# Performance work log

Hardware: AMD Instinct MI355X
Metric: run time of the kernel (lower is better)

## Reference

```python
import jax, jax.numpy as jnp
import numpy as np

DECAY = 0.99
EPS = 1e-05
COMMIT = 0.25


def setup_inputs() -> dict:
    key = jax.random.key(0)
    k1, k2 = jax.random.split(key)
    dim, n_embed = 256, 8192
    z = jax.random.normal(k1, (32, 32, 32, dim), dtype=jnp.float32)
    embed = jax.random.normal(k2, (dim, n_embed), dtype=jnp.float32)
    cluster_size = jnp.zeros((n_embed,), dtype=jnp.float32)
    embed_avg = embed  # torch init: embed_avg = embed.clone()
    return {"z": z, "embed": embed, "cluster_size": cluster_size, "embed_avg": embed_avg}


def reference(z, embed, cluster_size, embed_avg):
    dim, n_embed = embed.shape
    flatten = z.reshape(-1, dim)                       # [N, D]
    # squared L2 distance to each code: ||f||^2 - 2 f.E + ||E||^2
    dist = ((flatten ** 2).sum(1, keepdims=True)
            - 2.0 * flatten @ embed
            + (embed ** 2).sum(0, keepdims=True))      # [N, K]
    ind = jnp.argmin(dist, axis=1)                     # [N]
    quantize = jnp.take(embed.T, ind, axis=0).reshape(z.shape)
    embed_ind = ind.reshape(z.shape[:-1])

    # EMA codebook update (training mode), via segment_sum instead of a dense one-hot
    counts = jax.ops.segment_sum(jnp.ones_like(ind, dtype=flatten.dtype), ind,
                                 num_segments=n_embed)          # [K]
    embed_sum = jax.ops.segment_sum(flatten, ind,
                                    num_segments=n_embed).T     # [D, K]
    cluster_size_new = cluster_size * DECAY + (1.0 - DECAY) * counts
    embed_avg_new = embed_avg * DECAY + (1.0 - DECAY) * embed_sum
    n = cluster_size_new.sum()
    cs = (cluster_size_new + EPS) / (n + n_embed * EPS) * n
    embed_new = embed_avg_new / cs[None, :]

    diff = COMMIT * jnp.mean((jax.lax.stop_gradient(quantize) - z) ** 2)
    quantize_st = z + jax.lax.stop_gradient(quantize - z)  # straight-through
    return quantize_st, diff, embed_ind, embed_new
```

## Files before the change

### kernel.cpp

```cpp
#include <hip/hip_runtime.h>
#include <hip/hip_bf16.h>

#define D 256
#define K 8192
#define NTOT 32768
#define BM 128
#define BN2 128
#define BD 32
#define CSPLIT 4
#define CT_PER (K / CSPLIT / BN2)

typedef __bf16 bf16x8 __attribute__((ext_vector_type(8)));
typedef float f32x4 __attribute__((ext_vector_type(4)));

__device__ __forceinline__ void gl_lds16(const void* g, void* l) {
    __builtin_amdgcn_global_load_lds(
        (__attribute__((address_space(1))) void*)(g),
        (__attribute__((address_space(3))) void*)(l), 16, 0, 0);
}

__device__ __forceinline__ unsigned int enc_f32(float f) {
    unsigned int u = __float_as_uint(f);
    return (u & 0x80000000u) ? ~u : (u | 0x80000000u);
}

__device__ __forceinline__ unsigned short f2bfu(float x) {
    __hip_bfloat16 h = __float2bfloat16(x);
    return __builtin_bit_cast(unsigned short, h);
}
__device__ __forceinline__ float bfu2f(unsigned short u) {
    return __bfloat162float(__builtin_bit_cast(__hip_bfloat16, u));
}

__global__ __launch_bounds__(256)
void conv_F(const float* __restrict__ z, unsigned short* __restrict__ Fhi,
            unsigned short* __restrict__ Flo) {
    int i4 = blockIdx.x * 256 + threadIdx.x;
    float4 v = ((const float4*)z)[i4];
    ushort4 h, l;
    h.x = f2bfu(v.x); l.x = f2bfu(v.x - bfu2f(h.x));
    h.y = f2bfu(v.y); l.y = f2bfu(v.y - bfu2f(h.y));
    h.z = f2bfu(v.z); l.z = f2bfu(v.z - bfu2f(h.z));
    h.w = f2bfu(v.w); l.w = f2bfu(v.w - bfu2f(h.w));
    ((ushort4*)Fhi)[i4] = h;
    ((ushort4*)Flo)[i4] = l;
}

__global__ __launch_bounds__(256)
void conv_E(const float* __restrict__ E, unsigned short* __restrict__ EhiT,
            unsigned short* __restrict__ EloT, float* __restrict__ ET,
            float* __restrict__ enorm) {
    __shared__ float tile[64][65];
    int tid = threadIdx.x;
    int k0 = blockIdx.x * 64, d0 = blockIdx.y * 64;
#pragma unroll
    for (int it = 0; it < 16; ++it) {
        int idx = it * 256 + tid;
        int dr = idx >> 6, kc = idx & 63;
        tile[kc][dr] = E[(d0 + dr) * K + k0 + kc];
    }
    __syncthreads();
    float psum[4];
#pragma unroll
    for (int it = 0; it < 16; ++it) {
        int idx = it * 256 + tid;
        int kr = idx >> 6, dc = idx & 63;
        float v = tile[kr][dc];
        unsigned short h = f2bfu(v);
        int o = (k0 + kr) * D + d0 + dc;
        EhiT[o] = h;
        EloT[o] = f2bfu(v - bfu2f(h));
        ET[o] = v;
        psum[it & 3] = (it < 4 ? 0.f : psum[it & 3]) + v * v;
    }
#pragma unroll
    for (int g = 0; g < 4; ++g) {
        float p = psum[g];
#pragma unroll
        for (int off = 32; off; off >>= 1) p += __shfl_down(p, off);
        if ((tid & 63) == 0) {
            int kr = g * 4 + (tid >> 6);
            atomicAdd(&enorm[k0 + kr * 4 + 0], 0.f);
        }
    }
}

__global__ __launch_bounds__(256)
void enorm_kernel(const float* __restrict__ ET, float* __restrict__ enorm) {
    int k = blockIdx.x * 256 + threadIdx.x;
    const float4* row = (const float4*)(ET + k * D);
    float s = 0.f;
#pragma unroll
    for (int d = 0; d < D / 4; ++d) {
        float4 v = row[d];
        s += v.x * v.x + v.y * v.y + v.z * v.z + v.w * v.w;
    }
    enorm[k] = s;
}

__global__ __launch_bounds__(256)
void mfma_dist_argmin(const unsigned short* __restrict__ Fhi,
                      const unsigned short* __restrict__ Flo,
                      const unsigned short* __restrict__ EhiT,
                      const unsigned short* __restrict__ EloT,
                      const float* __restrict__ enorm,
                      unsigned long long* __restrict__ bestpack) {
    __shared__ unsigned short Ah[BM * BD], Al[BM * BD], Bh[BN2 * BD], Bl[BN2 * BD];

    const int tid = threadIdx.x;
    const int wave = tid >> 6;
    const int lane = tid & 63;
    const int qd = lane >> 4;
    const int ln = lane & 15;
    const int wm = (wave >> 1) * 64;
    const int wn = (wave & 1) * 64;
    const int n0 = blockIdx.x * BM;
    const int c0 = blockIdx.y * (K / CSPLIT);
    const int r_ = tid >> 2;
    const int s_sw = (tid & 3) ^ ((tid >> 3) & 3);
    const int csw = (qd ^ ((ln >> 1) & 3)) * 8;

    float bestv[16];
    int besti[16];
#pragma unroll
    for (int i = 0; i < 16; ++i) { bestv[i] = 3.402823466e38f; besti[i] = 0; }

    for (int ct = 0; ct < CT_PER; ++ct) {
        const int cb = c0 + ct * BN2;
        f32x4 acc[4][4];
#pragma unroll
        for (int mi = 0; mi < 4; ++mi)
#pragma unroll
            for (int ni = 0; ni < 4; ++ni) acc[mi][ni] = (f32x4){0.f, 0.f, 0.f, 0.f};

        for (int d0 = 0; d0 < D; d0 += BD) {
            __syncthreads();
#pragma unroll
            for (int it = 0; it < 2; ++it) {
                const int ga = (n0 + it * 64 + r_) * D + d0 + s_sw * 8;
                const int gb = (cb + it * 64 + r_) * D + d0 + s_sw * 8;
                const int lo = it * 2048 + wave * 512;
                gl_lds16(Fhi + ga, &Ah[lo]);
                gl_lds16(Flo + ga, &Al[lo]);
                gl_lds16(EhiT + gb, &Bh[lo]);
                gl_lds16(EloT + gb, &Bl[lo]);
            }
            __syncthreads();

            bf16x8 ah[4], al[4], bh[4], bl[4];
#pragma unroll
            for (int mi = 0; mi < 4; ++mi) {
                int off = (wm + mi * 16 + ln) * BD + csw;
                ah[mi] = *(const bf16x8*)&Ah[off];
                al[mi] = *(const bf16x8*)&Al[off];
            }
#pragma unroll
            for (int ni = 0; ni < 4; ++ni) {
                int off = (wn + ni * 16 + ln) * BD + csw;
                bh[ni] = *(const bf16x8*)&Bh[off];
                bl[ni] = *(const bf16x8*)&Bl[off];
            }
#pragma unroll
            for (int mi = 0; mi < 4; ++mi)
#pragma unroll
                for (int ni = 0; ni < 4; ++ni)
                    acc[mi][ni] = __builtin_amdgcn_mfma_f32_16x16x32_bf16(
                        ah[mi], bh[ni], acc[mi][ni], 0, 0, 0);
#pragma unroll
            for (int mi = 0; mi < 4; ++mi)
#pragma unroll
                for (int ni = 0; ni < 4; ++ni)
                    acc[mi][ni] = __builtin_amdgcn_mfma_f32_16x16x32_bf16(
                        ah[mi], bl[ni], acc[mi][ni], 0, 0, 0);
#pragma unroll
            for (int mi = 0; mi < 4; ++mi)
#pragma unroll
                for (int ni = 0; ni < 4; ++ni)
                    acc[mi][ni] = __builtin_amdgcn_mfma_f32_16x16x32_bf16(
                        al[mi], bh[ni], acc[mi][ni], 0, 0, 0);
        }

        float en[4];
#pragma unroll
        for (int ni = 0; ni < 4; ++ni) en[ni] = enorm[cb + wn + ni * 16 + ln];
#pragma unroll
        for (int ni = 0; ni < 4; ++ni) {
            int k = cb + wn + ni * 16 + ln;
#pragma unroll
            for (int mi = 0; mi < 4; ++mi) {
                f32x4 a = acc[mi][ni];
#pragma unroll
                for (int r = 0; r < 4; ++r) {
                    float dist = en[ni] - 2.0f * a[r];
                    int bi = mi * 4 + r;
                    if (dist < bestv[bi]) { bestv[bi] = dist; besti[bi] = k; }
                }
            }
        }
    }

#pragma unroll
    for (int mi = 0; mi < 4; ++mi) {
#pragma unroll
        for (int r = 0; r < 4; ++r) {
            int bi = mi * 4 + r;
            float v = bestv[bi];
            int ix = besti[bi];
#pragma unroll
            for (int off = 1; off < 16; off <<= 1) {
                float v2 = __shfl_xor(v, off);
                int i2 = __shfl_xor(ix, off);
                if (v2 < v || (v2 == v && i2 < ix)) { v = v2; ix = i2; }
            }
            if (ln == 0) {
                int m = n0 + wm + mi * 16 + qd * 4 + r;
                unsigned long long pack =
                    ((unsigned long long)enc_f32(v) << 32) | (unsigned int)ix;
                atomicMin(&bestpack[m], pack);
            }
        }
    }
}

#define ROWS_PER_BLOCK 64
__global__ __launch_bounds__(256)
void assign_apply(const float* __restrict__ z,
                  const float* __restrict__ ET,
                  const unsigned long long* __restrict__ bestpack,
                  float* __restrict__ out_q, float* __restrict__ out_ind,
                  float* __restrict__ out_diff,
                  float* __restrict__ counts, float* __restrict__ esumT) {
    const int tx = threadIdx.x;
    const int rbase = blockIdx.x * ROWS_PER_BLOCK;
    float part = 0.f;
    for (int r = 0; r < ROWS_PER_BLOCK; ++r) {
        int n = rbase + r;
        unsigned long long p = bestpack[n];
        int idx = (int)(p & 0xFFFFFFFFull);
        float f = z[n * D + tx];
        float q = ET[idx * D + tx];
        out_q[n * D + tx] = q;
        float dd = q - f;
        part += dd * dd;
        atomicAdd(&esumT[idx * D + tx], f);
        if (tx == 0) {
            atomicAdd(&counts[idx], 1.0f);
            out_ind[n] = (float)idx;
        }
    }
#pragma unroll
    for (int off = 32; off; off >>= 1) part += __shfl_down(part, off);
    __shared__ float wsum[4];
    if ((tx & 63) == 0) wsum[tx >> 6] = part;
    __syncthreads();
    if (tx == 0) {
        float t = wsum[0] + wsum[1] + wsum[2] + wsum[3];
        atomicAdd(out_diff, t * (0.25f / 8388608.0f));
    }
}

__global__ __launch_bounds__(1024)
void csn_sum(const float* __restrict__ cs_in, const float* __restrict__ counts,
             float* __restrict__ csn, float* __restrict__ nsum) {
    const float decay = 0.99f;
    const float omd = 0.01f;
    int tx = threadIdx.x;
    float p = 0.f;
    for (int k = tx; k < K; k += 1024) {
        float v = decay * cs_in[k] + omd * counts[k];
        csn[k] = v;
        p += v;
    }
#pragma unroll
    for (int off = 32; off; off >>= 1) p += __shfl_down(p, off);
    __shared__ float red[16];
    if ((tx & 63) == 0) red[tx >> 6] = p;
    __syncthreads();
    if (tx == 0) {
        float t = 0.f;
        for (int i = 0; i < 16; ++i) t += red[i];
        nsum[0] = t;
    }
}

__global__ __launch_bounds__(256)
void finalize(const float* __restrict__ eavg, const float* __restrict__ esumT,
              const float* __restrict__ csn, const float* __restrict__ nsum,
              float* __restrict__ out_enew) {
    const float decay = 0.99f;
    const float omd = 0.01f;
    const float keps = (float)(8192 * 1e-5);
    int idx = blockIdx.x * 256 + threadIdx.x;
    float nv = nsum[0];
    int k = idx & (K - 1);
    int d = idx >> 13;
    float avg_new = decay * eavg[idx] + omd * esumT[k * D + d];
    float cs = (csn[k] + 1e-5f) / (nv + keps) * nv;
    out_enew[idx] = avg_new / cs;
}

extern "C" void kernel_launch(void* const* d_in, const int* in_sizes, int n_in,
                              void* d_out, int out_size, void* d_ws, size_t ws_size,
                              hipStream_t stream) {
    const float* z = (const float*)d_in[0];
    const float* embed = (const float*)d_in[1];
    const float* cs_in = (const float*)d_in[2];
    const float* eavg = (const float*)d_in[3];

    float* out = (float*)d_out;
    float* out_q = out;
    float* out_diff = out + 8388608;
    float* out_ind = out + 8388609;
    float* out_enew = out + 8421377;

    char* ws = (char*)d_ws;
    unsigned long long* bestpack = (unsigned long long*)ws;
    float* enorm = (float*)(ws + 262144);
    float* counts = (float*)(ws + 294912);
    float* csn = (float*)(ws + 327680);
    float* nsum = (float*)(ws + 360448);
    float* esumT = (float*)(ws + 360704);
    unsigned short* Fhi = (unsigned short*)(ws + 8749312);
    unsigned short* Flo = (unsigned short*)(ws + 25526528);
    unsigned short* EhiT = (unsigned short*)(ws + 42303744);
    unsigned short* EloT = (unsigned short*)(ws + 46498048);
    float* ET = (float*)(ws + 50692352);

    hipMemsetAsync(bestpack, 0xFF, NTOT * 8, stream);
    hipMemsetAsync(counts, 0, K * 4, stream);
    hipMemsetAsync(esumT, 0, K * D * 4, stream);
    hipMemsetAsync(out_diff, 0, 4, stream);

    conv_F<<<NTOT * D / 4 / 256, 256, 0, stream>>>(z, Fhi, Flo);
    conv_E<<<dim3(K / 64, D / 64), 256, 0, stream>>>(embed, EhiT, EloT, ET, enorm);
    enorm_kernel<<<K / 256, 256, 0, stream>>>(ET, enorm);
    mfma_dist_argmin<<<dim3(NTOT / BM, CSPLIT), 256, 0, stream>>>(Fhi, Flo, EhiT, EloT,
                                                                  enorm, bestpack);
    assign_apply<<<NTOT / ROWS_PER_BLOCK, 256, 0, stream>>>(z, ET, bestpack, out_q,
                                                            out_ind, out_diff, counts, esumT);
    csn_sum<<<1, 1024, 0, stream>>>(cs_in, counts, csn, nsum);
    finalize<<<(D * K) / 256, 256, 0, stream>>>(eavg, esumT, csn, nsum, out_enew);
}
```

Measured before the change: 598.1 us.

## Load codebook fragments directly from global, shrink assign blocks, drop dead enorm atomics

In the distance GEMM kernel the B operand (codebook hi/lo bf16) is no longer staged through LDS. Each wave now reads its MFMA fragments straight from global memory into registers, which cuts LDS footprint and LDS traffic but duplicates global/L2 reads across the waves that share the same columns. Separately, conv_E drops its dead partial-norm reduction and zero-valued atomics, and assign_apply uses 16 rows per block with a partially unrolled loop to raise parallelism.

```diff
diff --git a/kernel.cpp b/kernel.cpp
--- a/kernel.cpp
+++ b/kernel.cpp
@@ -48,8 +48,7 @@
 
 __global__ __launch_bounds__(256)
 void conv_E(const float* __restrict__ E, unsigned short* __restrict__ EhiT,
-            unsigned short* __restrict__ EloT, float* __restrict__ ET,
-            float* __restrict__ enorm) {
+            unsigned short* __restrict__ EloT, float* __restrict__ ET) {
     __shared__ float tile[64][65];
     int tid = threadIdx.x;
     int k0 = blockIdx.x * 64, d0 = blockIdx.y * 64;
@@ -60,7 +59,6 @@
         tile[kc][dr] = E[(d0 + dr) * K + k0 + kc];
     }
     __syncthreads();
-    float psum[4];
 #pragma unroll
     for (int it = 0; it < 16; ++it) {
         int idx = it * 256 + tid;
@@ -71,17 +69,6 @@
         EhiT[o] = h;
         EloT[o] = f2bfu(v - bfu2f(h));
         ET[o] = v;
-        psum[it & 3] = (it < 4 ? 0.f : psum[it & 3]) + v * v;
-    }
-#pragma unroll
-    for (int g = 0; g < 4; ++g) {
-        float p = psum[g];
-#pragma unroll
-        for (int off = 32; off; off >>= 1) p += __shfl_down(p, off);
-        if ((tid & 63) == 0) {
-            int kr = g * 4 + (tid >> 6);
-            atomicAdd(&enorm[k0 + kr * 4 + 0], 0.f);
-        }
     }
 }
 
@@ -105,7 +92,7 @@
                       const unsigned short* __restrict__ EloT,
                       const float* __restrict__ enorm,
                       unsigned long long* __restrict__ bestpack) {
-    __shared__ unsigned short Ah[BM * BD], Al[BM * BD], Bh[BN2 * BD], Bl[BN2 * BD];
+    __shared__ unsigned short Ah[BM * BD], Al[BM * BD];
 
     const int tid = threadIdx.x;
     const int wave = tid >> 6;
@@ -120,6 +107,10 @@
     const int s_sw = (tid & 3) ^ ((tid >> 3) & 3);
     const int csw = (qd ^ ((ln >> 1) & 3)) * 8;
 
+    int boff[4];
+#pragma unroll
+    for (int ni = 0; ni < 4; ++ni) boff[ni] = (wn + ni * 16 + ln) * D + qd * 8;
+
     float bestv[16];
     int besti[16];
 #pragma unroll
@@ -138,27 +129,25 @@
 #pragma unroll
             for (int it = 0; it < 2; ++it) {
                 const int ga = (n0 + it * 64 + r_) * D + d0 + s_sw * 8;
-                const int gb = (cb + it * 64 + r_) * D + d0 + s_sw * 8;
                 const int lo = it * 2048 + wave * 512;
                 gl_lds16(Fhi + ga, &Ah[lo]);
                 gl_lds16(Flo + ga, &Al[lo]);
-                gl_lds16(EhiT + gb, &Bh[lo]);
-                gl_lds16(EloT + gb, &Bl[lo]);
+            }
+            const int sb = cb * D + d0;
+            bf16x8 bh[4], bl[4];
+#pragma unroll
+            for (int ni = 0; ni < 4; ++ni) {
+                bh[ni] = *(const bf16x8*)(EhiT + sb + boff[ni]);
+                bl[ni] = *(const bf16x8*)(EloT + sb + boff[ni]);
             }
             __syncthreads();
 
-            bf16x8 ah[4], al[4], bh[4], bl[4];
+            bf16x8 ah[4], al[4];
 #pragma unroll
             for (int mi = 0; mi < 4; ++mi) {
                 int off = (wm + mi * 16 + ln) * BD + csw;
                 ah[mi] = *(const bf16x8*)&Ah[off];
                 al[mi] = *(const bf16x8*)&Al[off];
-            }
-#pragma unroll
-            for (int ni = 0; ni < 4; ++ni) {
-                int off = (wn + ni * 16 + ln) * BD + csw;
-                bh[ni] = *(const bf16x8*)&Bh[off];
-                bl[ni] = *(const bf16x8*)&Bl[off];
             }
 #pragma unroll
             for (int mi = 0; mi < 4; ++mi)
@@ -222,7 +211,7 @@
     }
 }
 
-#define ROWS_PER_BLOCK 64
+#define ROWS_PER_BLOCK 16
 __global__ __launch_bounds__(256)
 void assign_apply(const float* __restrict__ z,
                   const float* __restrict__ ET,
@@ -233,6 +222,7 @@
     const int tx = threadIdx.x;
     const int rbase = blockIdx.x * ROWS_PER_BLOCK;
     float part = 0.f;
+#pragma unroll 4
     for (int r = 0; r < ROWS_PER_BLOCK; ++r) {
         int n = rbase + r;
         unsigned long long p = bestpack[n];
@@ -332,7 +322,7 @@
     hipMemsetAsync(out_diff, 0, 4, stream);
 
     conv_F<<<NTOT * D / 4 / 256, 256, 0, stream>>>(z, Fhi, Flo);
-    conv_E<<<dim3(K / 64, D / 64), 256, 0, stream>>>(embed, EhiT, EloT, ET, enorm);
+    conv_E<<<dim3(K / 64, D / 64), 256, 0, stream>>>(embed, EhiT, EloT, ET);
     enorm_kernel<<<K / 256, 256, 0, stream>>>(ET, enorm);
     mfma_dist_argmin<<<dim3(NTOT / BM, CSPLIT), 256, 0, stream>>>(Fhi, Flo, EhiT, EloT,
                                                                   enorm, bestpack);
```

Result: slower. 845.3 us (+41.3%).

## Fuse codebook norms into conversion, trim MFMA fragment registers, parallelize small kernels

Applied to the files above, without the earlier changes.

Codebook squared norms are now computed inside conv_E with wave shuffle reductions and atomics, so the separate enorm_kernel launch and its re-read of ET go away. The distance GEMM loop stages fewer bf16 fragments at once, reusing registers across the three split-precision MFMA passes, and hoists the LDS offsets out of the loop. assign_apply takes fewer rows per block and csn_sum runs across several blocks with an atomic total. The three workspace memsets are merged into one. The trade-off is extra atomics and a possible small change in floating-point summation order for the norms and the total.

```diff
diff --git a/kernel.cpp b/kernel.cpp
--- a/kernel.cpp
+++ b/kernel.cpp
@@ -60,7 +60,6 @@
         tile[kc][dr] = E[(d0 + dr) * K + k0 + kc];
     }
     __syncthreads();
-    float psum[4];
 #pragma unroll
     for (int it = 0; it < 16; ++it) {
         int idx = it * 256 + tid;
@@ -71,31 +70,11 @@
         EhiT[o] = h;
         EloT[o] = f2bfu(v - bfu2f(h));
         ET[o] = v;
-        psum[it & 3] = (it < 4 ? 0.f : psum[it & 3]) + v * v;
-    }
-#pragma unroll
-    for (int g = 0; g < 4; ++g) {
-        float p = psum[g];
+        float p = v * v;
 #pragma unroll
         for (int off = 32; off; off >>= 1) p += __shfl_down(p, off);
-        if ((tid & 63) == 0) {
-            int kr = g * 4 + (tid >> 6);
-            atomicAdd(&enorm[k0 + kr * 4 + 0], 0.f);
-        }
-    }
-}
-
-__global__ __launch_bounds__(256)
-void enorm_kernel(const float* __restrict__ ET, float* __restrict__ enorm) {
-    int k = blockIdx.x * 256 + threadIdx.x;
-    const float4* row = (const float4*)(ET + k * D);
-    float s = 0.f;
-#pragma unroll
-    for (int d = 0; d < D / 4; ++d) {
-        float4 v = row[d];
-        s += v.x * v.x + v.y * v.y + v.z * v.z + v.w * v.w;
-    }
-    enorm[k] = s;
+        if ((tid & 63) == 0) atomicAdd(&enorm[k0 + kr], p);
+    }
 }
 
 __global__ __launch_bounds__(256)
@@ -120,6 +99,12 @@
     const int s_sw = (tid & 3) ^ ((tid >> 3) & 3);
     const int csw = (qd ^ ((ln >> 1) & 3)) * 8;
 
+    int aro[4], bro[4];
+#pragma unroll
+    for (int mi = 0; mi < 4; ++mi) aro[mi] = (wm + mi * 16 + ln) * BD + csw;
+#pragma unroll
+    for (int ni = 0; ni < 4; ++ni) bro[ni] = (wn + ni * 16 + ln) * BD + csw;
+
     float bestv[16];
     int besti[16];
 #pragma unroll
@@ -147,51 +132,45 @@
             }
             __syncthreads();
 
-            bf16x8 ah[4], al[4], bh[4], bl[4];
-#pragma unroll
-            for (int mi = 0; mi < 4; ++mi) {
-                int off = (wm + mi * 16 + ln) * BD + csw;
-                ah[mi] = *(const bf16x8*)&Ah[off];
-                al[mi] = *(const bf16x8*)&Al[off];
-            }
-#pragma unroll
-            for (int ni = 0; ni < 4; ++ni) {
-                int off = (wn + ni * 16 + ln) * BD + csw;
-                bh[ni] = *(const bf16x8*)&Bh[off];
-                bl[ni] = *(const bf16x8*)&Bl[off];
-            }
+            bf16x8 a0[4], b0[4], b1[4];
+#pragma unroll
+            for (int mi = 0; mi < 4; ++mi) a0[mi] = *(const bf16x8*)&Ah[aro[mi]];
+#pragma unroll
+            for (int ni = 0; ni < 4; ++ni) b0[ni] = *(const bf16x8*)&Bh[bro[ni]];
 #pragma unroll
             for (int mi = 0; mi < 4; ++mi)
 #pragma unroll
                 for (int ni = 0; ni < 4; ++ni)
                     acc[mi][ni] = __builtin_amdgcn_mfma_f32_16x16x32_bf16(
-                        ah[mi], bh[ni], acc[mi][ni], 0, 0, 0);
+                        a0[mi], b0[ni], acc[mi][ni], 0, 0, 0);
+#pragma unroll
+            for (int ni = 0; ni < 4; ++ni) b1[ni] = *(const bf16x8*)&Bl[bro[ni]];
 #pragma unroll
             for (int mi = 0; mi < 4; ++mi)
 #pragma unroll
                 for (int ni = 0; ni < 4; ++ni)
                     acc[mi][ni] = __builtin_amdgcn_mfma_f32_16x16x32_bf16(
-                        ah[mi], bl[ni], acc[mi][ni], 0, 0, 0);
+                        a0[mi], b1[ni], acc[mi][ni], 0, 0, 0);
+#pragma unroll
+            for (int mi = 0; mi < 4; ++mi) a0[mi] = *(const bf16x8*)&Al[aro[mi]];
 #pragma unroll
             for (int mi = 0; mi < 4; ++mi)
 #pragma unroll
                 for (int ni = 0; ni < 4; ++ni)
                     acc[mi][ni] = __builtin_amdgcn_mfma_f32_16x16x32_bf16(
-                        al[mi], bh[ni], acc[mi][ni], 0, 0, 0);
+                        a0[mi], b0[ni], acc[mi][ni], 0, 0, 0);
         }
 
-        float en[4];
-#pragma unroll
-        for (int ni = 0; ni < 4; ++ni) en[ni] = enorm[cb + wn + ni * 16 + ln];
 #pragma unroll
         for (int ni = 0; ni < 4; ++ni) {
             int k = cb + wn + ni * 16 + ln;
+            float en = enorm[k];
 #pragma unroll
             for (int mi = 0; mi < 4; ++mi) {
                 f32x4 a = acc[mi][ni];
 #pragma unroll
                 for (int r = 0; r < 4; ++r) {
-                    float dist = en[ni] - 2.0f * a[r];
+                    float dist = en - 2.0f * a[r];
                     int bi = mi * 4 + r;
                     if (dist < bestv[bi]) { bestv[bi] = dist; besti[bi] = k; }
                 }
@@ -222,7 +201,7 @@
     }
 }
 
-#define ROWS_PER_BLOCK 64
+#define ROWS_PER_BLOCK 16
 __global__ __launch_bounds__(256)
 void assign_apply(const float* __restrict__ z,
                   const float* __restrict__ ET,
@@ -233,6 +212,7 @@
     const int tx = threadIdx.x;
     const int rbase = blockIdx.x * ROWS_PER_BLOCK;
     float part = 0.f;
+#pragma unroll 4
     for (int r = 0; r < ROWS_PER_BLOCK; ++r) {
         int n = rbase + r;
         unsigned long long p = bestpack[n];
@@ -264,22 +244,20 @@
              float* __restrict__ csn, float* __restrict__ nsum) {
     const float decay = 0.99f;
     const float omd = 0.01f;
-    int tx = threadIdx.x;
-    float p = 0.f;
-    for (int k = tx; k < K; k += 1024) {
-        float v = decay * cs_in[k] + omd * counts[k];
-        csn[k] = v;
-        p += v;
-    }
+    int k = blockIdx.x * 1024 + threadIdx.x;
+    float v = decay * cs_in[k] + omd * counts[k];
+    csn[k] = v;
+    float p = v;
 #pragma unroll
     for (int off = 32; off; off >>= 1) p += __shfl_down(p, off);
     __shared__ float red[16];
-    if ((tx & 63) == 0) red[tx >> 6] = p;
+    if ((threadIdx.x & 63) == 0) red[threadIdx.x >> 6] = p;
     __syncthreads();
-    if (tx == 0) {
+    if (threadIdx.x == 0) {
         float t = 0.f;
+#pragma unroll
         for (int i = 0; i < 16; ++i) t += red[i];
-        nsum[0] = t;
+        atomicAdd(nsum, t);
     }
 }
 
@@ -327,17 +305,15 @@
     float* ET = (float*)(ws + 50692352);
 
     hipMemsetAsync(bestpack, 0xFF, NTOT * 8, stream);
-    hipMemsetAsync(counts, 0, K * 4, stream);
-    hipMemsetAsync(esumT, 0, K * D * 4, stream);
+    hipMemsetAsync(ws + 262144, 0, 8749312 - 262144, stream);
     hipMemsetAsync(out_diff, 0, 4, stream);
 
     conv_F<<<NTOT * D / 4 / 256, 256, 0, stream>>>(z, Fhi, Flo);
     conv_E<<<dim3(K / 64, D / 64), 256, 0, stream>>>(embed, EhiT, EloT, ET, enorm);
-    enorm_kernel<<<K / 256, 256, 0, stream>>>(ET, enorm);
     mfma_dist_argmin<<<dim3(NTOT / BM, CSPLIT), 256, 0, stream>>>(Fhi, Flo, EhiT, EloT,
                                                                   enorm, bestpack);
     assign_apply<<<NTOT / ROWS_PER_BLOCK, 256, 0, stream>>>(z, ET, bestpack, out_q,
                                                             out_ind, out_diff, counts, esumT);
-    csn_sum<<<1, 1024, 0, stream>>>(cs_in, counts, csn, nsum);
+    csn_sum<<<K / 1024, 1024, 0, stream>>>(cs_in, counts, csn, nsum);
     finalize<<<(D * K) / 256, 256, 0, stream>>>(eavg, esumT, csn, nsum, out_enew);
 }
```

New measurement: 600.0 us. No clear change (+0.3%).
